# Optimization experiments

Hardware: AMD Instinct MI355X
Metric: run time of the kernel (lower is better)

The kernel has to match this reference:

```python
import jax, jax.numpy as jnp
import numpy as np

B, KPLUS1, D = 64, 513, 1024

def setup_inputs() -> dict:
    key = jax.random.key(0)
    k1, k2, k3 = jax.random.split(key, 3)
    x = jax.random.normal(k1, (B, KPLUS1, D), dtype=jnp.float32)
    # glorot-style scaled init for faithfulness in magnitude
    dense_weights = jax.random.normal(k2, (2 * D, D), dtype=jnp.float32) * (1.0 / np.sqrt(2 * D))
    dot_bias = jax.random.normal(k3, (D, 1), dtype=jnp.float32) * (1.0 / np.sqrt(D))
    return {"x": x, "dense_weights": dense_weights, "dot_bias": dot_bias}

def reference(x, dense_weights, dot_bias):
    # x: [B, K+1, D]; x[:,0] = sentence encoding u, x[:,1:] = knowledge z_t
    u = x[:, 0, :]            # [B, D]
    z = x[:, 1:, :]           # [B, K, D]
    d = z.shape[-1]
    # concat(z_t, u) @ W1 == z @ W1[:D] + u @ W1[D:], broadcast over K
    # (mathematically identical to the tile+concat+matmul in the original)
    w_z = dense_weights[:d, :]   # [D, D]
    w_u = dense_weights[d:, :]   # [D, D]
    m = jnp.tanh(jnp.einsum('bkd,de->bke', z, w_z)
                 + jnp.einsum('bd,de->be', u, w_u)[:, None, :])  # [B, K, D]
    q = jnp.einsum('bke,e->bk', m, dot_bias[:, 0])               # [B, K]
    return jax.nn.softmax(q, axis=-1)                            # [B, K]
```

## Files before the change

kernel.cpp:

```cpp
#include <hip/hip_runtime.h>
#include <hip/hip_bf16.h>


typedef __attribute__((ext_vector_type(8))) short short8;
typedef __attribute__((ext_vector_type(8))) _Float16 half8;
typedef __attribute__((ext_vector_type(4))) float f32x4;
typedef unsigned short ushort_t;

typedef const __attribute__((address_space(1))) void gvoid_t;
typedef __attribute__((address_space(3))) void lvoid_t;

__device__ __forceinline__ ushort_t f2bf(float f) {
    unsigned u = __float_as_uint(f);
    unsigned r = u + 0x7FFFu + ((u >> 16) & 1u);
    return (ushort_t)(r >> 16);
}
__device__ __forceinline__ float bf2f(ushort_t h) {
    return __uint_as_float(((unsigned)h) << 16);
}
__device__ __forceinline__ float tanh_fast(float x) {
    float e = __expf(2.f * x);
    return 1.f - 2.f / (e + 1.f);
}

__global__ __launch_bounds__(256) void k_prep_all2(const float* __restrict__ x,
                                                   const float* __restrict__ w,
                                                   _Float16* __restrict__ z_h,
                                                   _Float16* __restrict__ wzt,
                                                   float* __restrict__ hu) {
    __shared__ float us[1024];
    __shared__ _Float16 th[64][66];
    const int blk = blockIdx.x;
    const int t = threadIdx.x;

    if (blk < 256) {
        const int b = blk >> 2;
        const int e = (blk & 3) * 256 + t;
        for (int i = t; i < 1024; i += 256)
            us[i] = x[(size_t)b * 513 * 1024 + i];
        __syncthreads();
        const float* wu = w + (size_t)1024 * 1024;
        float acc = 0.f;
#pragma unroll 8
        for (int d = 0; d < 1024; ++d)
            acc = fmaf(us[d], wu[(size_t)d * 1024 + e], acc);
        hu[b * 1024 + e] = acc;
    } else if (blk < 512) {
        const int idx = blk - 256;
        const int k0 = (idx & 15) * 64;
        const int n0 = (idx >> 4) * 64;
        const int lr = t >> 6;
        const int lc = t & 63;
#pragma unroll
        for (int r = 0; r < 16; ++r) {
            int kk = r * 4 + lr;
            th[kk][lc] = (_Float16)w[(size_t)(k0 + kk) * 1024 + n0 + lc];
        }
        __syncthreads();
#pragma unroll
        for (int r = 0; r < 16; ++r) {
            int nn = r * 4 + lr;
            wzt[(size_t)(n0 + nn) * 1024 + k0 + lc] = th[lc][nn];
        }
    } else {
        const int idx8 = (blk - 512) * 256 + t;
        const int m = idx8 >> 7;
        const int c = (idx8 & 127) * 8;
        const int b = m >> 9, k = m & 511;
        const float* src = x + ((size_t)(b * 513 + 1 + k) << 10) + c;
        const float4 v0 = *(const float4*)src;
        const float4 v1 = *(const float4*)(src + 4);
        half8 hv;
        hv[0] = (_Float16)v0.x; hv[1] = (_Float16)v0.y;
        hv[2] = (_Float16)v0.z; hv[3] = (_Float16)v0.w;
        hv[4] = (_Float16)v1.x; hv[5] = (_Float16)v1.y;
        hv[6] = (_Float16)v1.z; hv[7] = (_Float16)v1.w;
        *(half8*)(z_h + (size_t)m * 1024 + c) = hv;
    }
}

__global__ __launch_bounds__(512) void k_gemm13(
        const _Float16* __restrict__ z_h,
        const _Float16* __restrict__ wzt,
        const float* __restrict__ hu,
        const float* __restrict__ bias,
        float* __restrict__ qp) {
    __shared__ __align__(16) _Float16 lds[3 * 16384];
    __shared__ float qred[2][4][128];

    const int t = threadIdx.x;
    const int mtile = blockIdx.x;
    const int ntile = blockIdx.y;
    const int wid = t >> 6;
    const int l = t & 63;
    const int wm = wid >> 2;
    const int wn = wid & 3;
    const int lr = l & 15;
    const int g = l >> 4;

    char* ldsb = (char*)lds;

    const int swz = (g ^ ((lr >> 1) & 3)) * 16;
    const int aOffRd = (wm * 128 + lr) * 64 + swz;
    const int bOffRd = 16384 + (wn * 64 + lr) * 64 + swz;

    const int schunk = ((t & 3) ^ ((t >> 3) & 3)) * 8;
    size_t aSrc[2], bSrc[2];
#pragma unroll
    for (int j = 0; j < 2; ++j) {
        aSrc[j] = (size_t)(mtile * 256 + (t >> 2) + j * 128) * 1024 + schunk;
        bSrc[j] = (size_t)(ntile * 256 + (t >> 2) + j * 128) * 1024 + schunk;
    }

#define STAGE(kt, SLOT)                                                      \
    {   const int _kc = (kt) * 32;                                           \
        char* _d = ldsb + (SLOT) * 32768;                                    \
        _Pragma("unroll")                                                    \
        for (int j = 0; j < 2; ++j)                                          \
            __builtin_amdgcn_global_load_lds((gvoid_t*)(z_h + aSrc[j] + _kc),\
                (lvoid_t*)(_d + t * 16 + j * 8192), 16, 0, 0);               \
        _Pragma("unroll")                                                    \
        for (int j = 0; j < 2; ++j)                                          \
            __builtin_amdgcn_global_load_lds((gvoid_t*)(wzt + bSrc[j] + _kc),\
                (lvoid_t*)(_d + 16384 + t * 16 + j * 8192), 16, 0, 0); }

#define KBODY(T, SLOT, DOSTAGE, VMSTR)                                       \
    {   char* _sb = ldsb + (SLOT) * 32768;                                   \
        half8 afr[8], bfr[4];                                                \
        _Pragma("unroll")                                                    \
        for (int ni = 0; ni < 4; ++ni)                                       \
            bfr[ni] = *(const half8*)(_sb + bOffRd + ni * 1024);             \
        _Pragma("unroll")                                                    \
        for (int mi = 0; mi < 8; ++mi)                                       \
            afr[mi] = *(const half8*)(_sb + aOffRd + mi * 1024);             \
        if (DOSTAGE) { STAGE((T) + 2, ((SLOT) + 2) % 3); }                   \
        asm volatile("s_waitcnt lgkmcnt(0)" ::: "memory");                   \
        __builtin_amdgcn_sched_barrier(0);                                   \
        __builtin_amdgcn_s_setprio(1);                                       \
        _Pragma("unroll")                                                    \
        for (int mi = 0; mi < 8; ++mi)                                       \
            _Pragma("unroll")                                                \
            for (int ni = 0; ni < 4; ++ni)                                   \
                acc[mi][ni] = __builtin_amdgcn_mfma_f32_16x16x32_f16(        \
                    afr[mi], bfr[ni], acc[mi][ni], 0, 0, 0);                 \
        __builtin_amdgcn_s_setprio(0);                                       \
        asm volatile(VMSTR ::: "memory");                                    \
        __builtin_amdgcn_sched_barrier(0);                                   \
        __builtin_amdgcn_s_barrier(); }

    f32x4 acc[8][4] = {};

    STAGE(0, 0); STAGE(1, 1);
    asm volatile("s_waitcnt vmcnt(4)" ::: "memory");
    __builtin_amdgcn_sched_barrier(0);
    __builtin_amdgcn_s_barrier();

#pragma unroll 1
    for (int i = 0; i < 10; ++i) {
        const int T = i * 3;
        KBODY(T + 0, 0, true, "s_waitcnt vmcnt(4)");
        KBODY(T + 1, 1, true, "s_waitcnt vmcnt(4)");
        KBODY(T + 2, 2, true, "s_waitcnt vmcnt(4)");
    }
    KBODY(30, 0, false, "s_waitcnt vmcnt(0)");
    KBODY(31, 1, false, "s_nop 0");
#undef KBODY
#undef STAGE

    const int bb = mtile >> 1;
    float hu4[4], bias4[4];
#pragma unroll
    for (int ni = 0; ni < 4; ++ni) {
        int e = ntile * 256 + wn * 64 + ni * 16 + lr;
        hu4[ni] = hu[bb * 1024 + e];
        bias4[ni] = bias[e];
    }
#pragma unroll
    for (int mi = 0; mi < 8; ++mi) {
#pragma unroll
        for (int j = 0; j < 4; ++j) {
            float v = 0.f;
#pragma unroll
            for (int ni = 0; ni < 4; ++ni)
                v += tanh_fast(acc[mi][ni][j] + hu4[ni]) * bias4[ni];
            v += __shfl_xor(v, 1);
            v += __shfl_xor(v, 2);
            v += __shfl_xor(v, 4);
            v += __shfl_xor(v, 8);
            if (lr == 0)
                qred[wm][wn][mi * 16 + g * 4 + j] = v;
        }
    }
    __syncthreads();
    if (t < 256) {
        const int wmr = t >> 7;
        const int rr = t & 127;
        float q = qred[wmr][0][rr] + qred[wmr][1][rr]
                + qred[wmr][2][rr] + qred[wmr][3][rr];
        qp[(size_t)ntile * 32768 + mtile * 256 + t] = q;
    }
}

__global__ void k_prep_w(const float* __restrict__ w,
                         ushort_t* __restrict__ wzt_hi,
                         ushort_t* __restrict__ wzt_lo) {
    __shared__ ushort_t th[64][66];
    __shared__ ushort_t tl[64][66];
    const int k0 = blockIdx.x * 64;
    const int n0 = blockIdx.y * 64;
    const int t = threadIdx.x;
    const int lr = t >> 6;
    const int lc = t & 63;
#pragma unroll
    for (int r = 0; r < 16; ++r) {
        int kk = r * 4 + lr;
        float f = w[(size_t)(k0 + kk) * 1024 + n0 + lc];
        ushort_t hi = f2bf(f);
        ushort_t lo = f2bf(f - bf2f(hi));
        th[kk][lc] = hi;
        tl[kk][lc] = lo;
    }
    __syncthreads();
#pragma unroll
    for (int r = 0; r < 16; ++r) {
        int nn = r * 4 + lr;
        wzt_hi[(size_t)(n0 + nn) * 1024 + k0 + lc] = th[lc][nn];
        wzt_lo[(size_t)(n0 + nn) * 1024 + k0 + lc] = tl[lc][nn];
    }
}

__global__ void k_hu(const float* __restrict__ x,
                     const float* __restrict__ w,
                     float* __restrict__ hu) {
    __shared__ float us[1024];
    const int b = blockIdx.y;
    const int e = blockIdx.x * 256 + threadIdx.x;
    for (int i = threadIdx.x; i < 1024; i += 256)
        us[i] = x[(size_t)b * 513 * 1024 + i];
    __syncthreads();
    const float* wu = w + (size_t)1024 * 1024;
    float acc = 0.f;
#pragma unroll 8
    for (int d = 0; d < 1024; ++d)
        acc = fmaf(us[d], wu[(size_t)d * 1024 + e], acc);
    hu[b * 1024 + e] = acc;
}

__global__ __launch_bounds__(256) void k_gemm(
        const float* __restrict__ x,
        const ushort_t* __restrict__ wzt_hi,
        const ushort_t* __restrict__ wzt_lo,
        const float* __restrict__ hu,
        const float* __restrict__ bias,
        float* __restrict__ qp) {
    __shared__ ushort_t As_hi[128][40];
    __shared__ ushort_t As_lo[128][40];
    __shared__ ushort_t Bs_hi[128][40];
    __shared__ ushort_t Bs_lo[128][40];
    __shared__ float qred[2][2][64];

    const int t = threadIdx.x;
    const int mtile = blockIdx.x;
    const int ntile = blockIdx.y;
    const int wid = t >> 6;
    const int l = t & 63;
    const int wm = wid >> 1;
    const int wn = wid & 1;

    f32x4 acc[4][4] = {};

    const int arow = t >> 3;
    const int acol = (t & 7) * 4;
    size_t abase[4];
#pragma unroll
    for (int it = 0; it < 4; ++it) {
        int m = mtile * 128 + arow + it * 32;
        int bb = m >> 9;
        int kk = m & 511;
        abase[it] = ((size_t)(bb * 513 + 1 + kk)) * 1024 + acol;
    }
    const int brow = t >> 2;
    const int bcol = (t & 3) * 8;
    const size_t bbase = (size_t)(ntile * 128 + brow) * 1024 + bcol;

    for (int k0 = 0; k0 < 1024; k0 += 32) {
#pragma unroll
        for (int it = 0; it < 4; ++it) {
            const float4 v = *(const float4*)(x + abase[it] + k0);
            ushort4 hv, lv;
            hv.x = f2bf(v.x); lv.x = f2bf(v.x - bf2f(hv.x));
            hv.y = f2bf(v.y); lv.y = f2bf(v.y - bf2f(hv.y));
            hv.z = f2bf(v.z); lv.z = f2bf(v.z - bf2f(hv.z));
            hv.w = f2bf(v.w); lv.w = f2bf(v.w - bf2f(hv.w));
            const int row = arow + it * 32;
            *(ushort4*)&As_hi[row][acol] = hv;
            *(ushort4*)&As_lo[row][acol] = lv;
        }
#pragma unroll
        for (int it = 0; it < 2; ++it) {
            const int row = brow + it * 64;
            const uint4 vh = *(const uint4*)(wzt_hi + bbase + (size_t)it * 64 * 1024 + k0);
            const uint4 vl = *(const uint4*)(wzt_lo + bbase + (size_t)it * 64 * 1024 + k0);
            *(uint4*)&Bs_hi[row][bcol] = vh;
            *(uint4*)&Bs_lo[row][bcol] = vl;
        }
        __syncthreads();

        const int lr = l & 15;
        const int lk = (l >> 4) * 8;
        short8 ah[4], al[4], bh[4], bl[4];
#pragma unroll
        for (int i = 0; i < 4; ++i) {
            ah[i] = *(const short8*)&As_hi[wm * 64 + i * 16 + lr][lk];
            al[i] = *(const short8*)&As_lo[wm * 64 + i * 16 + lr][lk];
            bh[i] = *(const short8*)&Bs_hi[wn * 64 + i * 16 + lr][lk];
            bl[i] = *(const short8*)&Bs_lo[wn * 64 + i * 16 + lr][lk];
        }
#pragma unroll
        for (int mi = 0; mi < 4; ++mi)
#pragma unroll
            for (int ni = 0; ni < 4; ++ni) {
                acc[mi][ni] = __builtin_amdgcn_mfma_f32_16x16x32_bf16(ah[mi], bh[ni], acc[mi][ni], 0, 0, 0);
                acc[mi][ni] = __builtin_amdgcn_mfma_f32_16x16x32_bf16(ah[mi], bl[ni], acc[mi][ni], 0, 0, 0);
                acc[mi][ni] = __builtin_amdgcn_mfma_f32_16x16x32_bf16(al[mi], bh[ni], acc[mi][ni], 0, 0, 0);
            }
        __syncthreads();
    }

    const int lr = l & 15;
    const int lg = l >> 4;
    const int bbatch = mtile >> 2;
    float hu4[4], bias4[4];
#pragma unroll
    for (int ni = 0; ni < 4; ++ni) {
        int e = ntile * 128 + wn * 64 + ni * 16 + lr;
        hu4[ni] = hu[bbatch * 1024 + e];
        bias4[ni] = bias[e];
    }
#pragma unroll
    for (int mi = 0; mi < 4; ++mi) {
#pragma unroll
        for (int j = 0; j < 4; ++j) {
            float v = 0.f;
#pragma unroll
            for (int ni = 0; ni < 4; ++ni)
                v += tanhf(acc[mi][ni][j] + hu4[ni]) * bias4[ni];
            v += __shfl_xor(v, 1);
            v += __shfl_xor(v, 2);
            v += __shfl_xor(v, 4);
            v += __shfl_xor(v, 8);
            if (lr == 0)
                qred[wm][wn][mi * 16 + lg * 4 + j] = v;
        }
    }
    __syncthreads();
    if (t < 128) {
        const int wmr = t >> 6;
        const int rr = t & 63;
        float qv = qred[wmr][0][rr] + qred[wmr][1][rr];
        qp[(size_t)ntile * 32768 + mtile * 128 + t] = qv;
    }
}

__global__ void k_softmax(const float* __restrict__ qp, float* __restrict__ out,
                          int nt) {
    const int b = blockIdx.x;
    const int k = threadIdx.x;
    float q = 0.f;
    for (int i = 0; i < nt; ++i)
        q += qp[(size_t)i * 32768 + b * 512 + k];

    __shared__ float redm[8];
    __shared__ float reds[8];
    const int wid = k >> 6;

    float m = q;
#pragma unroll
    for (int off = 32; off >= 1; off >>= 1)
        m = fmaxf(m, __shfl_xor(m, off));
    if ((k & 63) == 0) redm[wid] = m;
    __syncthreads();
    m = redm[0];
#pragma unroll
    for (int i = 1; i < 8; ++i) m = fmaxf(m, redm[i]);

    float p = expf(q - m);
    float s = p;
#pragma unroll
    for (int off = 32; off >= 1; off >>= 1)
        s += __shfl_xor(s, off);
    if ((k & 63) == 0) reds[wid] = s;
    __syncthreads();
    s = 0.f;
#pragma unroll
    for (int i = 0; i < 8; ++i) s += reds[i];

    out[b * 512 + k] = p / s;
}

extern "C" void kernel_launch(void* const* d_in, const int* in_sizes, int n_in,
                              void* d_out, int out_size, void* d_ws, size_t ws_size,
                              hipStream_t stream) {
    const float* x    = (const float*)d_in[0];
    const float* w    = (const float*)d_in[1];
    const float* bias = (const float*)d_in[2];
    float* out = (float*)d_out;

    char* ws = (char*)d_ws;
    const size_t ZN = (size_t)32768 * 1024;

    const size_t need = ZN * sizeof(_Float16)
                      + (size_t)1024 * 1024 * sizeof(_Float16)
                      + (size_t)64 * 1024 * sizeof(float)
                      + (size_t)4 * 32768 * sizeof(float);

    if (ws_size >= need) {
        _Float16* z_h = (_Float16*)ws;
        _Float16* wzt = z_h + ZN;
        float*    hu  = (float*)(wzt + (size_t)1024 * 1024);
        float*    qp  = hu + (size_t)64 * 1024;

        k_prep_all2<<<16896, 256, 0, stream>>>(x, w, z_h, wzt, hu);
        k_gemm13<<<dim3(128, 4), 512, 0, stream>>>(z_h, wzt, hu, bias, qp);
        k_softmax<<<64, 512, 0, stream>>>(qp, out, 4);
    } else {
        ushort_t* wzt_hi = (ushort_t*)ws;
        ushort_t* wzt_lo = wzt_hi + (size_t)1024 * 1024;
        float* hu = (float*)(ws + (size_t)4 * 1024 * 1024);
        float* qp = hu + (size_t)64 * 1024;

        k_prep_w<<<dim3(16, 16), 256, 0, stream>>>(w, wzt_hi, wzt_lo);
        k_hu<<<dim3(4, 64), 256, 0, stream>>>(x, w, hu);
        k_gemm<<<dim3(256, 8), 256, 0, stream>>>(x, wzt_hi, wzt_lo, hu, bias, qp);
        k_softmax<<<64, 512, 0, stream>>>(qp, out, 8);
    }
}
```

Baseline: 165.7 us.

## Use four LDS stages with paired k-steps and one barrier per pair

The GEMM main loop goes from a triple-buffered LDS pipeline with a barrier after every 32-wide k-step to a quad-buffered scheme. Each iteration stages two future k-tiles, computes two k-steps, then waits on all loads and synchronises once. The aim is to halve the number of barriers and keep more loads in flight per iteration. In exchange LDS use grows from 96KB to 128KB per block. Draining vmcnt to zero every iteration may expose load latency more than the old vmcnt(4) scheme did.

```diff
diff --git a/kernel.cpp b/kernel.cpp
--- a/kernel.cpp
+++ b/kernel.cpp
@@ -79,13 +79,13 @@
     }
 }
 
-__global__ __launch_bounds__(512) void k_gemm13(
+__global__ __launch_bounds__(512) void k_gemm16(
         const _Float16* __restrict__ z_h,
         const _Float16* __restrict__ wzt,
         const float* __restrict__ hu,
         const float* __restrict__ bias,
         float* __restrict__ qp) {
-    __shared__ __align__(16) _Float16 lds[3 * 16384];
+    __shared__ __align__(16) _Float16 lds[4 * 16384];
     __shared__ float qred[2][4][128];
 
     const int t = threadIdx.x;
@@ -112,9 +112,9 @@
         bSrc[j] = (size_t)(ntile * 256 + (t >> 2) + j * 128) * 1024 + schunk;
     }
 
-#define STAGE(kt, SLOT)                                                      \
+#define STAGE(kt)                                                            \
     {   const int _kc = (kt) * 32;                                           \
-        char* _d = ldsb + (SLOT) * 32768;                                    \
+        char* _d = ldsb + ((kt) & 3) * 32768;                                \
         _Pragma("unroll")                                                    \
         for (int j = 0; j < 2; ++j)                                          \
             __builtin_amdgcn_global_load_lds((gvoid_t*)(z_h + aSrc[j] + _kc),\
@@ -124,7 +124,7 @@
             __builtin_amdgcn_global_load_lds((gvoid_t*)(wzt + bSrc[j] + _kc),\
                 (lvoid_t*)(_d + 16384 + t * 16 + j * 8192), 16, 0, 0); }
 
-#define KBODY(T, SLOT, DOSTAGE, VMSTR)                                       \
+#define SUBSTEP(SLOT)                                                        \
     {   char* _sb = ldsb + (SLOT) * 32768;                                   \
         half8 afr[8], bfr[4];                                                \
         _Pragma("unroll")                                                    \
@@ -133,7 +133,6 @@
         _Pragma("unroll")                                                    \
         for (int mi = 0; mi < 8; ++mi)                                       \
             afr[mi] = *(const half8*)(_sb + aOffRd + mi * 1024);             \
-        if (DOSTAGE) { STAGE((T) + 2, ((SLOT) + 2) % 3); }                   \
         asm volatile("s_waitcnt lgkmcnt(0)" ::: "memory");                   \
         __builtin_amdgcn_sched_barrier(0);                                   \
         __builtin_amdgcn_s_setprio(1);                                       \
@@ -143,28 +142,26 @@
             for (int ni = 0; ni < 4; ++ni)                                   \
                 acc[mi][ni] = __builtin_amdgcn_mfma_f32_16x16x32_f16(        \
                     afr[mi], bfr[ni], acc[mi][ni], 0, 0, 0);                 \
-        __builtin_amdgcn_s_setprio(0);                                       \
-        asm volatile(VMSTR ::: "memory");                                    \
-        __builtin_amdgcn_sched_barrier(0);                                   \
-        __builtin_amdgcn_s_barrier(); }
+        __builtin_amdgcn_s_setprio(0); }
 
     f32x4 acc[8][4] = {};
 
-    STAGE(0, 0); STAGE(1, 1);
-    asm volatile("s_waitcnt vmcnt(4)" ::: "memory");
+    STAGE(0); STAGE(1);
+    asm volatile("s_waitcnt vmcnt(0)" ::: "memory");
     __builtin_amdgcn_sched_barrier(0);
     __builtin_amdgcn_s_barrier();
 
 #pragma unroll 1
-    for (int i = 0; i < 10; ++i) {
-        const int T = i * 3;
-        KBODY(T + 0, 0, true, "s_waitcnt vmcnt(4)");
-        KBODY(T + 1, 1, true, "s_waitcnt vmcnt(4)");
-        KBODY(T + 2, 2, true, "s_waitcnt vmcnt(4)");
-    }
-    KBODY(30, 0, false, "s_waitcnt vmcnt(0)");
-    KBODY(31, 1, false, "s_nop 0");
-#undef KBODY
+    for (int P = 0; P < 16; ++P) {
+        const int s0 = 2 * P;
+        if (P < 15) { STAGE(s0 + 2); STAGE(s0 + 3); }
+        SUBSTEP((s0) & 3)
+        SUBSTEP((s0 + 1) & 3)
+        asm volatile("s_waitcnt vmcnt(0)" ::: "memory");
+        __builtin_amdgcn_sched_barrier(0);
+        __builtin_amdgcn_s_barrier();
+    }
+#undef SUBSTEP
 #undef STAGE
 
     const int bb = mtile >> 1;
@@ -421,7 +418,7 @@
         float*    qp  = hu + (size_t)64 * 1024;
 
         k_prep_all2<<<16896, 256, 0, stream>>>(x, w, z_h, wzt, hu);
-        k_gemm13<<<dim3(128, 4), 512, 0, stream>>>(z_h, wzt, hu, bias, qp);
+        k_gemm16<<<dim3(128, 4), 512, 0, stream>>>(z_h, wzt, hu, bias, qp);
         k_softmax<<<64, 512, 0, stream>>>(qp, out, 4);
     } else {
         ushort_t* wzt_hi = (ushort_t*)ws;
```

Result: slower. 173.4 us (+4.6%).
